# Kernel tuning notes

Measured on AMD Instinct MI355X. Metric: run time of the kernel, lower is better.

The kernel has to match this reference:

```python
import jax, jax.numpy as jnp
import numpy as np

B, D, C, T, DEPTH = 4096, 1024, 1000, 32, 6
N_INTERNAL = 2 ** DEPTH - 1
N_LEAVES = 2 ** DEPTH


def setup_inputs() -> dict:
    key = jax.random.key(0)
    k0, k1, k2 = jax.random.split(key, 3)
    x = jax.random.normal(k0, (B, D), jnp.float32)
    split_weights = jax.random.normal(k1, (T, N_INTERNAL, D), jnp.float32) * 0.1
    split_biases = jnp.zeros((T, N_INTERNAL), jnp.float32)
    leaf_logits = jax.random.normal(k2, (T, N_LEAVES, C), jnp.float32) * 0.1
    tree_weights = jnp.ones((T,), jnp.float32) / T
    log_temperature = jnp.zeros((), jnp.float32)
    return {
        "x": x,
        "split_weights": split_weights,
        "split_biases": split_biases,
        "leaf_logits": leaf_logits,
        "tree_weights": tree_weights,
        "log_temperature": log_temperature,
    }


def reference(x, split_weights, split_biases, leaf_logits, tree_weights, log_temperature):
    depth = int(np.log2(leaf_logits.shape[1]))
    temp = jnp.clip(jnp.exp(log_temperature), 0.1, 5.0)
    # split probabilities for all trees at once: [B, T, I]
    logits = jnp.einsum('bd,tid->bti', x, split_weights) + split_biases[None, :, :]
    s = jax.nn.sigmoid(logits / temp)
    b, t, _ = s.shape
    # iterative-doubling path probabilities; BFS leaf order matches the
    # original per-leaf loop (left child multiplies (1-s), right multiplies s)
    mu = jnp.ones((b, t, 1), s.dtype)
    for d in range(depth):
        lvl = s[:, :, 2 ** d - 1: 2 ** (d + 1) - 1]  # [B, T, 2^d] level-d splits
        mu = jnp.stack([mu * (1.0 - lvl), mu * lvl], axis=-1).reshape(b, t, 2 ** (d + 1))
    leaf_class_probs = jax.nn.softmax(leaf_logits / temp, axis=-1)  # [T, L, C]
    w = jax.nn.softmax(tree_weights, axis=0)                        # [T]
    # fused tree-weighted blend, avoids materializing [B, T, C]
    return jnp.einsum('btl,t,tlc->bc', mu, w, leaf_class_probs)
```

## Files before the change

### kernel.cpp

```cpp
#include <hip/hip_runtime.h>
#include <cstdint>
#include <cstddef>

constexpr int Bv = 4096;
constexpr int Dv = 1024;
constexpr int Cv = 1000;
constexpr int Tv = 32;
constexpr int NI = 63;
constexpr int NL = 64;
constexpr int TNp = 2048;
constexpr int TL = Tv * NL;
constexpr int Npad = 1024;

typedef _Float16 h8  __attribute__((ext_vector_type(8)));
typedef _Float16 h4  __attribute__((ext_vector_type(4)));
typedef short    s8v __attribute__((ext_vector_type(8)));
typedef unsigned short us8 __attribute__((ext_vector_type(8)));
typedef float    f4v __attribute__((ext_vector_type(4)));

constexpr size_t N_X    = (size_t)Bv * Dv;
constexpr size_t N_W    = (size_t)TNp * Dv;
constexpr size_t OFF_XH = 64;
constexpr size_t OFF_WH = OFF_XH + N_X / 2;
constexpr size_t OFF_P  = OFF_WH + N_W / 2;
constexpr size_t OFF_MH = OFF_P + (size_t)TL * Cv;
constexpr size_t OFF_PTH= OFF_MH + (size_t)Bv * TL / 2;

__device__ __forceinline__ unsigned short f2bf_rn(float x) {
    unsigned u = __float_as_uint(x);
    return (unsigned short)((u + 0x7fffu + ((u >> 16) & 1u)) >> 16);
}

__device__ __forceinline__ void gll16(const void* gptr, void* lptr) {
    __builtin_amdgcn_global_load_lds(
        (const __attribute__((address_space(1))) unsigned int*)gptr,
        (__attribute__((address_space(3))) unsigned int*)lptr,
        16, 0, 0);
}

__global__ __launch_bounds__(256)
void k_prep_leaf(const float* __restrict__ x, const float* __restrict__ sw,
                 const float* __restrict__ ll, const float* __restrict__ lt,
                 _Float16* __restrict__ Xh, _Float16* __restrict__ Wh,
                 float* __restrict__ P) {
    const int b = blockIdx.x;
    const int tid = threadIdx.x;
    if (b < 4096) {
        const size_t i4 = ((size_t)b * 256 + tid) * 4;
        const float4 v = *reinterpret_cast<const float4*>(&x[i4]);
        h4 vh;
        vh[0] = (_Float16)v.x; vh[1] = (_Float16)v.y;
        vh[2] = (_Float16)v.z; vh[3] = (_Float16)v.w;
        *reinterpret_cast<h4*>(&Xh[i4]) = vh;
    } else if (b < 6144) {
        const size_t d4 = ((size_t)(b - 4096) * 256 + tid) * 4;
        const int row = (int)(d4 >> 10);
        const int col = (int)(d4 & 1023);
        const int t = row >> 6, i = row & 63;
        float4 v = make_float4(0.f, 0.f, 0.f, 0.f);
        if (i < NI)
            v = *reinterpret_cast<const float4*>(&sw[(size_t)(t * NI + i) * Dv + col]);
        h4 vh;
        vh[0] = (_Float16)v.x; vh[1] = (_Float16)v.y;
        vh[2] = (_Float16)v.z; vh[3] = (_Float16)v.w;
        *reinterpret_cast<h4*>(&Wh[d4]) = vh;
    } else {
        const int r = b - 6144;
        const float temp = fminf(fmaxf(expf(lt[0]), 0.1f), 5.0f);
        const float invT = 1.0f / temp;
        const float* row = ll + (size_t)r * Cv;
        float* pr = P + (size_t)r * Cv;
        __shared__ float redm[4];
        __shared__ float reds[4];

        float m = -3.4e38f;
        for (int c = tid; c < Cv; c += 256) m = fmaxf(m, row[c] * invT);
        #pragma unroll
        for (int o = 32; o > 0; o >>= 1) m = fmaxf(m, __shfl_down(m, o));
        if ((tid & 63) == 0) redm[tid >> 6] = m;
        __syncthreads();
        m = fmaxf(fmaxf(redm[0], redm[1]), fmaxf(redm[2], redm[3]));

        float sum = 0.f;
        for (int c = tid; c < Cv; c += 256) {
            const float e = expf(row[c] * invT - m);
            pr[c] = e;
            sum += e;
        }
        #pragma unroll
        for (int o = 32; o > 0; o >>= 1) sum += __shfl_down(sum, o);
        if ((tid & 63) == 0) reds[tid >> 6] = sum;
        __syncthreads();
        sum = reds[0] + reds[1] + reds[2] + reds[3];
        const float rs = 1.0f / sum;
        for (int c = tid; c < Cv; c += 256) pr[c] *= rs;
    }
}

__global__ __launch_bounds__(256, 4)
void k_gemm1mu_tp(const _Float16* __restrict__ Xh, const _Float16* __restrict__ Wh,
                  const float* __restrict__ bias, const float* __restrict__ tw,
                  const float* __restrict__ lt, const float* __restrict__ P,
                  unsigned short* __restrict__ MH, unsigned short* __restrict__ PTH) {
    __shared__ __align__(16) char lds[33280];

    const int tid = threadIdx.x;

    if (blockIdx.x >= 512) {
        const int tpb = blockIdx.x - 512;
        const int k0 = (tpb & 31) * 64;
        const int c0 = (tpb >> 5) * 64;
        float* T = (float*)lds;
        #pragma unroll
        for (int i = 0; i < 16; ++i) {
            const int idx = tid + i * 256;
            const int kk = idx >> 6, cc = idx & 63;
            const int c = c0 + cc;
            T[kk * 65 + cc] = (c < Cv) ? P[(size_t)(k0 + kk) * Cv + c] : 0.f;
        }
        __syncthreads();
        #pragma unroll
        for (int i = 0; i < 16; ++i) {
            const int idx = tid + i * 256;
            const int cc = idx >> 6, kk = idx & 63;
            PTH[(size_t)(c0 + cc) * TL + k0 + kk] = f2bf_rn(T[kk * 65 + cc]);
        }
        return;
    }

    const int wg  = (blockIdx.x & 7) * 64 + (blockIdx.x >> 3);
    const int blk = wg >> 6;
    const int j   = wg & 63;
    const int bx  = (blk & 3) * 4 + (j & 3);
    const int by  = (blk >> 2) * 16 + (j >> 2);
    const int bm = by * 128, bn = bx * 128;

    const int lane = tid & 63, wv = tid >> 6;
    const int wr = wv >> 1, wc = wv & 1;
    const int lrow = lane & 15, kg = (lane >> 4) * 8;
    const int sr = lane >> 2;
    const int sc = (lane & 3) * 8;

    const float temp = fminf(fmaxf(expf(lt[0]), 0.1f), 5.0f);
    const float invT = 1.0f / temp;
    const int mytree = 2 * bx + wc;
    float wm = -3.4e38f;
    #pragma unroll
    for (int t = 0; t < Tv; ++t) wm = fmaxf(wm, tw[t]);
    float wsum = 0.f, wmine = 0.f;
    #pragma unroll
    for (int t = 0; t < Tv; ++t) {
        const float e = expf(tw[t] - wm);
        wsum += e;
        if (t == mytree) wmine = e;
    }
    const float wt = wmine / wsum;

    f4v acc[4][4] = {};

#define STG(bufi, k0)                                                         \
    { _Pragma("unroll")                                                       \
      for (int i_ = 0; i_ < 2; ++i_) {                                        \
        const int ch_  = wv * 2 + i_;                                         \
        const int row_ = ch_ * 16 + sr;                                       \
        gll16(&Xh[(size_t)(bm + row_) * Dv + (k0) + sc],                      \
              lds + (bufi) * 16384 + ch_ * 1024);                             \
        gll16(&Wh[(size_t)(bn + row_) * Dv + (k0) + sc],                      \
              lds + (bufi) * 16384 + 8192 + ch_ * 1024);                      \
      } }

    STG(0, 0);
    for (int t = 0; t < 32; ++t) {
        const int cur = t & 1;
        if (t < 31) {
            STG(cur ^ 1, (t + 1) * 32);
            asm volatile("s_waitcnt vmcnt(4)" ::: "memory");
        } else {
            asm volatile("s_waitcnt vmcnt(0)" ::: "memory");
        }
        __builtin_amdgcn_s_barrier();
        __builtin_amdgcn_sched_barrier(0);

        h8 a[4], b[4];
        #pragma unroll
        for (int mf = 0; mf < 4; ++mf)
            a[mf] = *reinterpret_cast<const h8*>(
                lds + cur * 16384 + ((wr * 64 + mf * 16 + lrow) * 32 + kg) * 2);
        #pragma unroll
        for (int nf = 0; nf < 4; ++nf)
            b[nf] = *reinterpret_cast<const h8*>(
                lds + cur * 16384 + 8192 + ((wc * 64 + nf * 16 + lrow) * 32 + kg) * 2);
        #pragma unroll
        for (int mf = 0; mf < 4; ++mf)
            #pragma unroll
            for (int nf = 0; nf < 4; ++nf)
                acc[mf][nf] = __builtin_amdgcn_mfma_f32_16x16x32_f16(a[mf], b[nf], acc[mf][nf], 0, 0, 0);

        __builtin_amdgcn_sched_barrier(0);
        asm volatile("s_waitcnt lgkmcnt(0)" ::: "memory");
        __builtin_amdgcn_s_barrier();
    }
#undef STG

    _Float16* scr = (_Float16*)lds + wv * (64 * 65);
    #pragma unroll
    for (int nf = 0; nf < 4; ++nf) {
        const int colB = nf * 16 + lrow;
        const int gcol = bn + wc * 64 + colB;
        const int ii = gcol & 63;
        const float bv = (ii < NI) ? bias[(gcol >> 6) * NI + ii] : 0.f;
        #pragma unroll
        for (int mf = 0; mf < 4; ++mf) {
            #pragma unroll
            for (int r = 0; r < 4; ++r) {
                const int rowB = mf * 16 + (lane >> 4) * 4 + r;
                const float z = (acc[mf][nf][r] + bv) * invT;
                scr[rowB * 65 + colB] = (_Float16)(1.0f / (1.0f + __expf(-z)));
            }
        }
    }
    asm volatile("s_waitcnt lgkmcnt(0)" ::: "memory");

    const _Float16* srow = scr + lane * 65;
    float mu[NL];
    mu[0] = wt;
    #pragma unroll
    for (int d = 0; d < 6; ++d) {
        const int width = 1 << d;
        #pragma unroll
        for (int i = width - 1; i >= 0; --i) {
            const float sv = (float)srow[width - 1 + i];
            const float m  = mu[i];
            mu[2 * i + 1] = m * sv;
            mu[2 * i]     = m * (1.0f - sv);
        }
    }
    const size_t obase = (size_t)(bm + wr * 64 + lane) * TL + (size_t)mytree * 64;
    #pragma unroll
    for (int c = 0; c < 8; ++c) {
        us8 vh;
        #pragma unroll
        for (int jj = 0; jj < 8; ++jj) vh[jj] = f2bf_rn(mu[c * 8 + jj]);
        *reinterpret_cast<us8*>(&MH[obase + c * 8]) = vh;
    }
}

__global__ __launch_bounds__(256, 2)
void k_gemm2(const unsigned short* __restrict__ MH, const unsigned short* __restrict__ PTH,
             float* __restrict__ out) {
    __shared__ unsigned short LA[2][2][128][32];
    __shared__ unsigned short LB[2][2][64][32];

    const int tid  = threadIdx.x;
    const int wg  = (blockIdx.x & 7) * 64 + (blockIdx.x >> 3);
    const int blk = wg >> 6;
    const int j   = wg & 63;
    const int bnt = (blk & 1) * 8 + (j & 7);
    const int bmt = (blk >> 1) * 8 + (j >> 3);
    const int bm = bmt * 128, bn = bnt * 64;

    const int lane = tid & 63;
    const int wv   = tid >> 6;
    const int wr   = wv >> 1;
    const int wc   = wv & 1;
    const int lrow = lane & 15;
    const int kg   = (lane >> 4) * 8;
    const int sr   = lane >> 2;
    const int sc   = (lane & 3) * 8;

    f4v acc[4][2] = {};

#define STAGE2(bufi, k0)                                                          \
    { _Pragma("unroll")                                                           \
      for (int kh_ = 0; kh_ < 2; ++kh_) {                                         \
        _Pragma("unroll")                                                         \
        for (int i_ = 0; i_ < 2; ++i_) {                                          \
          const int ch_  = wv * 2 + i_;                                           \
          const int row_ = ch_ * 16 + sr;                                         \
          gll16(&MH[(size_t)(bm + row_) * TL + (k0) + kh_ * 32 + sc],             \
                (char*)&LA[bufi][kh_][0][0] + ch_ * 1024);                        \
        }                                                                         \
        { const int row_ = wv * 16 + sr;                                          \
          gll16(&PTH[(size_t)(bn + row_) * TL + (k0) + kh_ * 32 + sc],            \
                (char*)&LB[bufi][kh_][0][0] + wv * 1024); }                       \
      } }

    STAGE2(0, 0);
    for (int t = 0; t < 32; ++t) {
        const int cur = t & 1;
        if (t < 31) {
            STAGE2(cur ^ 1, (t + 1) * 64);
            asm volatile("s_waitcnt vmcnt(6)" ::: "memory");
        } else {
            asm volatile("s_waitcnt vmcnt(0)" ::: "memory");
        }
        __builtin_amdgcn_s_barrier();
        __builtin_amdgcn_sched_barrier(0);

        #pragma unroll
        for (int kh = 0; kh < 2; ++kh) {
            s8v a[4], b[2];
            #pragma unroll
            for (int mf = 0; mf < 4; ++mf)
                a[mf] = *reinterpret_cast<const s8v*>(&LA[cur][kh][wr * 64 + mf * 16 + lrow][kg]);
            #pragma unroll
            for (int nf = 0; nf < 2; ++nf)
                b[nf] = *reinterpret_cast<const s8v*>(&LB[cur][kh][wc * 32 + nf * 16 + lrow][kg]);
            #pragma unroll
            for (int mf = 0; mf < 4; ++mf)
                #pragma unroll
                for (int nf = 0; nf < 2; ++nf)
                    acc[mf][nf] = __builtin_amdgcn_mfma_f32_16x16x32_bf16(a[mf], b[nf], acc[mf][nf], 0, 0, 0);
        }

        __builtin_amdgcn_sched_barrier(0);
        asm volatile("s_waitcnt lgkmcnt(0)" ::: "memory");
        __builtin_amdgcn_s_barrier();
    }
#undef STAGE2

    #pragma unroll
    for (int nf = 0; nf < 2; ++nf) {
        const int col = bn + wc * 32 + nf * 16 + lrow;
        if (col >= Cv) continue;
        #pragma unroll
        for (int mf = 0; mf < 4; ++mf) {
            #pragma unroll
            for (int r = 0; r < 4; ++r) {
                const int row = bm + wr * 64 + mf * 16 + (lane >> 4) * 4 + r;
                out[(size_t)row * Cv + col] = acc[mf][nf][r];
            }
        }
    }
}

extern "C" void kernel_launch(void* const* d_in, const int* in_sizes, int n_in,
                              void* d_out, int out_size, void* d_ws, size_t ws_size,
                              hipStream_t stream) {
    const float* x  = (const float*)d_in[0];
    const float* sw = (const float*)d_in[1];
    const float* sb = (const float*)d_in[2];
    const float* ll = (const float*)d_in[3];
    const float* tw = (const float*)d_in[4];
    const float* lt = (const float*)d_in[5];

    float* out  = (float*)d_out;
    float* ws   = (float*)d_ws;
    _Float16* Xh = (_Float16*)(ws + OFF_XH);
    _Float16* Wh = (_Float16*)(ws + OFF_WH);
    float* Pbuf = ws + OFF_P;
    unsigned short* MH  = (unsigned short*)(ws + OFF_MH);
    unsigned short* PTH = (unsigned short*)(ws + OFF_PTH);

    k_prep_leaf<<<8192, 256, 0, stream>>>(x, sw, ll, lt, Xh, Wh, Pbuf);
    k_gemm1mu_tp<<<1024, 256, 0, stream>>>(Xh, Wh, sb, tw, lt, Pbuf, MH, PTH);
    k_gemm2<<<512, 256, 0, stream>>>(MH, PTH, out);
}
```

Measured before the change: 82.51 us.

## Fuse leaf softmax with bf16 transpose and split-K inside gemm2 waves

The leaf softmax now processes 8 rows per block in LDS and writes the transposed bf16 PTH matrix directly. This removes the fp32 P intermediate and the separate transpose blocks that previously ran in the gemm1 kernel. Gemm2 is restructured so each wave covers the full 64-column tile but only half of each 64-wide K chunk. The two K halves are reduced through LDS before the store, which raises MFMA work per LDS fragment load. The cost is a larger LDS footprint for gemm2 and a final cross-wave reduction with an extra sync, while prep blocks use 32KB LDS, which may lower their occupancy.

```diff
diff --git a/kernel.cpp b/kernel.cpp
--- a/kernel.cpp
+++ b/kernel.cpp
@@ -22,8 +22,7 @@
 constexpr size_t N_W    = (size_t)TNp * Dv;
 constexpr size_t OFF_XH = 64;
 constexpr size_t OFF_WH = OFF_XH + N_X / 2;
-constexpr size_t OFF_P  = OFF_WH + N_W / 2;
-constexpr size_t OFF_MH = OFF_P + (size_t)TL * Cv;
+constexpr size_t OFF_MH = OFF_WH + N_W / 2;
 constexpr size_t OFF_PTH= OFF_MH + (size_t)Bv * TL / 2;
 
 __device__ __forceinline__ unsigned short f2bf_rn(float x) {
@@ -42,7 +41,9 @@
 void k_prep_leaf(const float* __restrict__ x, const float* __restrict__ sw,
                  const float* __restrict__ ll, const float* __restrict__ lt,
                  _Float16* __restrict__ Xh, _Float16* __restrict__ Wh,
-                 float* __restrict__ P) {
+                 unsigned short* __restrict__ PTH) {
+    __shared__ __align__(16) char lds[8 * 1024 * 4 + 32];
+
     const int b = blockIdx.x;
     const int tid = threadIdx.x;
     if (b < 4096) {
@@ -65,69 +66,60 @@
         vh[2] = (_Float16)v.z; vh[3] = (_Float16)v.w;
         *reinterpret_cast<h4*>(&Wh[d4]) = vh;
     } else {
-        const int r = b - 6144;
+        const int blk = b - 6144;
+        const int r0 = blk * 8;
         const float temp = fminf(fmaxf(expf(lt[0]), 0.1f), 5.0f);
         const float invT = 1.0f / temp;
-        const float* row = ll + (size_t)r * Cv;
-        float* pr = P + (size_t)r * Cv;
-        __shared__ float redm[4];
-        __shared__ float reds[4];
-
-        float m = -3.4e38f;
-        for (int c = tid; c < Cv; c += 256) m = fmaxf(m, row[c] * invT);
-        #pragma unroll
-        for (int o = 32; o > 0; o >>= 1) m = fmaxf(m, __shfl_down(m, o));
-        if ((tid & 63) == 0) redm[tid >> 6] = m;
+        float* T  = (float*)lds;
+        float* rs = (float*)(lds + 8 * 1024 * 4);
+
+        #pragma unroll
+        for (int rr = 0; rr < 8; ++rr) {
+            for (int c = tid; c < 1024; c += 256)
+                T[rr * 1024 + c] = (c < Cv) ? ll[(size_t)(r0 + rr) * Cv + c] * invT
+                                            : -3.4e38f;
+        }
         __syncthreads();
-        m = fmaxf(fmaxf(redm[0], redm[1]), fmaxf(redm[2], redm[3]));
-
-        float sum = 0.f;
-        for (int c = tid; c < Cv; c += 256) {
-            const float e = expf(row[c] * invT - m);
-            pr[c] = e;
-            sum += e;
-        }
-        #pragma unroll
-        for (int o = 32; o > 0; o >>= 1) sum += __shfl_down(sum, o);
-        if ((tid & 63) == 0) reds[tid >> 6] = sum;
+
+        const int wv = tid >> 6, lane = tid & 63;
+        #pragma unroll
+        for (int rw = 0; rw < 2; ++rw) {
+            const int rr = wv * 2 + rw;
+            float m = -3.4e38f;
+            for (int c = lane; c < 1024; c += 64) m = fmaxf(m, T[rr * 1024 + c]);
+            #pragma unroll
+            for (int o = 32; o > 0; o >>= 1) m = fmaxf(m, __shfl_xor(m, o));
+            float s = 0.f;
+            for (int c = lane; c < 1024; c += 64) {
+                const float e = __expf(T[rr * 1024 + c] - m);
+                T[rr * 1024 + c] = e;
+                s += e;
+            }
+            #pragma unroll
+            for (int o = 32; o > 0; o >>= 1) s += __shfl_xor(s, o);
+            if (lane == 0) rs[rr] = 1.0f / s;
+        }
         __syncthreads();
-        sum = reds[0] + reds[1] + reds[2] + reds[3];
-        const float rs = 1.0f / sum;
-        for (int c = tid; c < Cv; c += 256) pr[c] *= rs;
+
+        for (int c = tid; c < 1024; c += 256) {
+            us8 v;
+            #pragma unroll
+            for (int rr = 0; rr < 8; ++rr) {
+                const float f = (c < Cv) ? T[rr * 1024 + c] * rs[rr] : 0.f;
+                v[rr] = f2bf_rn(f);
+            }
+            *reinterpret_cast<us8*>(&PTH[(size_t)c * TL + r0]) = v;
+        }
     }
 }
 
 __global__ __launch_bounds__(256, 4)
-void k_gemm1mu_tp(const _Float16* __restrict__ Xh, const _Float16* __restrict__ Wh,
-                  const float* __restrict__ bias, const float* __restrict__ tw,
-                  const float* __restrict__ lt, const float* __restrict__ P,
-                  unsigned short* __restrict__ MH, unsigned short* __restrict__ PTH) {
+void k_gemm1mu(const _Float16* __restrict__ Xh, const _Float16* __restrict__ Wh,
+               const float* __restrict__ bias, const float* __restrict__ tw,
+               const float* __restrict__ lt, unsigned short* __restrict__ MH) {
     __shared__ __align__(16) char lds[33280];
 
     const int tid = threadIdx.x;
-
-    if (blockIdx.x >= 512) {
-        const int tpb = blockIdx.x - 512;
-        const int k0 = (tpb & 31) * 64;
-        const int c0 = (tpb >> 5) * 64;
-        float* T = (float*)lds;
-        #pragma unroll
-        for (int i = 0; i < 16; ++i) {
-            const int idx = tid + i * 256;
-            const int kk = idx >> 6, cc = idx & 63;
-            const int c = c0 + cc;
-            T[kk * 65 + cc] = (c < Cv) ? P[(size_t)(k0 + kk) * Cv + c] : 0.f;
-        }
-        __syncthreads();
-        #pragma unroll
-        for (int i = 0; i < 16; ++i) {
-            const int idx = tid + i * 256;
-            const int cc = idx >> 6, kk = idx & 63;
-            PTH[(size_t)(c0 + cc) * TL + k0 + kk] = f2bf_rn(T[kk * 65 + cc]);
-        }
-        return;
-    }
-
     const int wg  = (blockIdx.x & 7) * 64 + (blockIdx.x >> 3);
     const int blk = wg >> 6;
     const int j   = wg & 63;
@@ -248,8 +240,7 @@
 __global__ __launch_bounds__(256, 2)
 void k_gemm2(const unsigned short* __restrict__ MH, const unsigned short* __restrict__ PTH,
              float* __restrict__ out) {
-    __shared__ unsigned short LA[2][2][128][32];
-    __shared__ unsigned short LB[2][2][64][32];
+    __shared__ __align__(16) char lds[49152];
 
     const int tid  = threadIdx.x;
     const int wg  = (blockIdx.x & 7) * 64 + (blockIdx.x >> 3);
@@ -262,34 +253,35 @@
     const int lane = tid & 63;
     const int wv   = tid >> 6;
     const int wr   = wv >> 1;
-    const int wc   = wv & 1;
+    const int wk   = wv & 1;
     const int lrow = lane & 15;
     const int kg   = (lane >> 4) * 8;
-    const int sr   = lane >> 2;
-    const int sc   = (lane & 3) * 8;
-
-    f4v acc[4][2] = {};
-
-#define STAGE2(bufi, k0)                                                          \
-    { _Pragma("unroll")                                                           \
-      for (int kh_ = 0; kh_ < 2; ++kh_) {                                         \
-        _Pragma("unroll")                                                         \
-        for (int i_ = 0; i_ < 2; ++i_) {                                          \
-          const int ch_  = wv * 2 + i_;                                           \
-          const int row_ = ch_ * 16 + sr;                                         \
-          gll16(&MH[(size_t)(bm + row_) * TL + (k0) + kh_ * 32 + sc],             \
-                (char*)&LA[bufi][kh_][0][0] + ch_ * 1024);                        \
-        }                                                                         \
-        { const int row_ = wv * 16 + sr;                                          \
-          gll16(&PTH[(size_t)(bn + row_) * TL + (k0) + kh_ * 32 + sc],            \
-                (char*)&LB[bufi][kh_][0][0] + wv * 1024); }                       \
+    const int sr   = lane >> 3;
+    const int sc   = (lane & 7) * 8;
+
+    f4v acc[4][4] = {};
+
+#define STG2(bufi, k0)                                                        \
+    { _Pragma("unroll")                                                       \
+      for (int i_ = 0; i_ < 4; ++i_) {                                        \
+        const int ch_  = wv * 4 + i_;                                         \
+        const int row_ = ch_ * 8 + sr;                                        \
+        gll16(&MH[(size_t)(bm + row_) * TL + (k0) + sc],                      \
+              lds + (bufi) * 24576 + ch_ * 1024);                             \
+      }                                                                       \
+      _Pragma("unroll")                                                       \
+      for (int i_ = 0; i_ < 2; ++i_) {                                        \
+        const int ch_  = wv * 2 + i_;                                         \
+        const int row_ = ch_ * 8 + sr;                                        \
+        gll16(&PTH[(size_t)(bn + row_) * TL + (k0) + sc],                     \
+              lds + (bufi) * 24576 + 16384 + ch_ * 1024);                     \
       } }
 
-    STAGE2(0, 0);
+    STG2(0, 0);
     for (int t = 0; t < 32; ++t) {
         const int cur = t & 1;
         if (t < 31) {
-            STAGE2(cur ^ 1, (t + 1) * 64);
+            STG2(cur ^ 1, (t + 1) * 64);
             asm volatile("s_waitcnt vmcnt(6)" ::: "memory");
         } else {
             asm volatile("s_waitcnt vmcnt(0)" ::: "memory");
@@ -297,38 +289,54 @@
         __builtin_amdgcn_s_barrier();
         __builtin_amdgcn_sched_barrier(0);
 
-        #pragma unroll
-        for (int kh = 0; kh < 2; ++kh) {
-            s8v a[4], b[2];
-            #pragma unroll
-            for (int mf = 0; mf < 4; ++mf)
-                a[mf] = *reinterpret_cast<const s8v*>(&LA[cur][kh][wr * 64 + mf * 16 + lrow][kg]);
-            #pragma unroll
-            for (int nf = 0; nf < 2; ++nf)
-                b[nf] = *reinterpret_cast<const s8v*>(&LB[cur][kh][wc * 32 + nf * 16 + lrow][kg]);
-            #pragma unroll
-            for (int mf = 0; mf < 4; ++mf)
-                #pragma unroll
-                for (int nf = 0; nf < 2; ++nf)
-                    acc[mf][nf] = __builtin_amdgcn_mfma_f32_16x16x32_bf16(a[mf], b[nf], acc[mf][nf], 0, 0, 0);
-        }
+        s8v a[4], bfr[4];
+        #pragma unroll
+        for (int mf = 0; mf < 4; ++mf)
+            a[mf] = *reinterpret_cast<const s8v*>(
+                lds + cur * 24576 + ((wr * 64 + mf * 16 + lrow) * 64 + wk * 32 + kg) * 2);
+        #pragma unroll
+        for (int nf = 0; nf < 4; ++nf)
+            bfr[nf] = *reinterpret_cast<const s8v*>(
+                lds + cur * 24576 + 16384 + ((nf * 16 + lrow) * 64 + wk * 32 + kg) * 2);
+        #pragma unroll
+        for (int mf = 0; mf < 4; ++mf)
+            #pragma unroll
+            for (int nf = 0; nf < 4; ++nf)
+                acc[mf][nf] = __builtin_amdgcn_mfma_f32_16x16x32_bf16(a[mf], bfr[nf], acc[mf][nf], 0, 0, 0);
 
         __builtin_amdgcn_sched_barrier(0);
         asm volatile("s_waitcnt lgkmcnt(0)" ::: "memory");
         __builtin_amdgcn_s_barrier();
     }
-#undef STAGE2
-
-    #pragma unroll
-    for (int nf = 0; nf < 2; ++nf) {
-        const int col = bn + wc * 32 + nf * 16 + lrow;
-        if (col >= Cv) continue;
-        #pragma unroll
-        for (int mf = 0; mf < 4; ++mf) {
-            #pragma unroll
-            for (int r = 0; r < 4; ++r) {
-                const int row = bm + wr * 64 + mf * 16 + (lane >> 4) * 4 + r;
-                out[(size_t)row * Cv + col] = acc[mf][nf][r];
+#undef STG2
+
+    float* red = (float*)lds;
+    if (wk == 1) {
+        #pragma unroll
+        for (int mf = 0; mf < 4; ++mf)
+            #pragma unroll
+            for (int nf = 0; nf < 4; ++nf)
+                #pragma unroll
+                for (int r = 0; r < 4; ++r) {
+                    const int rowB = mf * 16 + (lane >> 4) * 4 + r;
+                    const int colB = nf * 16 + lrow;
+                    red[wr * 4096 + rowB * 64 + colB] = acc[mf][nf][r];
+                }
+    }
+    __syncthreads();
+    if (wk == 0) {
+        #pragma unroll
+        for (int nf = 0; nf < 4; ++nf) {
+            const int col = bn + nf * 16 + lrow;
+            if (col >= Cv) continue;
+            #pragma unroll
+            for (int mf = 0; mf < 4; ++mf) {
+                #pragma unroll
+                for (int r = 0; r < 4; ++r) {
+                    const int rowB = mf * 16 + (lane >> 4) * 4 + r;
+                    const float v = acc[mf][nf][r] + red[wr * 4096 + rowB * 64 + nf * 16 + lrow];
+                    out[(size_t)(bm + wr * 64 + rowB) * Cv + col] = v;
+                }
             }
         }
     }
@@ -348,11 +356,10 @@
     float* ws   = (float*)d_ws;
     _Float16* Xh = (_Float16*)(ws + OFF_XH);
     _Float16* Wh = (_Float16*)(ws + OFF_WH);
-    float* Pbuf = ws + OFF_P;
     unsigned short* MH  = (unsigned short*)(ws + OFF_MH);
     unsigned short* PTH = (unsigned short*)(ws + OFF_PTH);
 
-    k_prep_leaf<<<8192, 256, 0, stream>>>(x, sw, ll, lt, Xh, Wh, Pbuf);
-    k_gemm1mu_tp<<<1024, 256, 0, stream>>>(Xh, Wh, sb, tw, lt, Pbuf, MH, PTH);
+    k_prep_leaf<<<6400, 256, 0, stream>>>(x, sw, ll, lt, Xh, Wh, PTH);
+    k_gemm1mu<<<512, 256, 0, stream>>>(Xh, Wh, sb, tw, lt, MH);
     k_gemm2<<<512, 256, 0, stream>>>(MH, PTH, out);
 }
```

After: 89.37 us. 8.3% more time.
